# Performance work log

Measured on AMD Instinct MI355X. Metric: run time of the kernel, lower is better.

The kernel has to match this reference:

```python
import jax, jax.numpy as jnp
import numpy as np

N_NODES = 50000
N_EDGES = 800000
D_IN = 96
D_OUT = 96


def setup_inputs() -> dict:
    key = jax.random.key(0)
    k1, k2, k3 = jax.random.split(key, 3)
    x = jax.random.normal(k1, (N_NODES, D_IN), dtype=jnp.float32)
    edge_index = jax.random.randint(k2, (2, N_EDGES), 0, N_NODES, dtype=jnp.int64)
    edge_weight = jnp.ones((N_EDGES,), dtype=jnp.float32)
    # Glorot-ish init for the linear weight, zero bias (as in PyG GCNConv)
    W = jax.random.normal(k3, (D_IN, D_OUT), dtype=jnp.float32) * (1.0 / np.sqrt(D_IN))
    b = jnp.zeros((D_OUT,), dtype=jnp.float32)
    return {"x": x, "edge_index": edge_index, "edge_weight": edge_weight, "W": W, "b": b}


def reference(x, edge_index, edge_weight, W, b):
    """PyG GCNConv: out = D^{-1/2} (A + I) D^{-1/2} (x @ W) + b."""
    N = x.shape[0]
    row, col = edge_index[0], edge_index[1]  # source -> target
    # add self loops with weight 1 (PyG default add_self_loops=True)
    loop = jnp.arange(N, dtype=edge_index.dtype)
    row = jnp.concatenate([row, loop])
    col = jnp.concatenate([col, loop])
    ew = jnp.concatenate([edge_weight, jnp.ones((N,), dtype=edge_weight.dtype)])
    # symmetric normalization based on (weighted) in-degree over col
    deg = jax.ops.segment_sum(ew, col, num_segments=N)  # [N]
    dinv = jnp.where(deg > 0, jax.lax.rsqrt(deg), 0.0)
    norm = dinv[row] * ew * dinv[col]  # [E+N]
    # linear transform first (small GEMM), then gather-scale-scatter over edges
    h = x @ W  # [N, D_OUT]
    msg = h[row] * norm[:, None]  # [E+N, D_OUT]
    out = jax.ops.segment_sum(msg, col, num_segments=N)  # [N, D_OUT]
    return out + b
```

## Files before the change

kernel.cpp:

```cpp
#include <hip/hip_runtime.h>

#define N_NODES 50000
#define N_EDGES 800000
#define D 96
#define NBKT 512
#define BNODES 98
#define BCAP 2304
#define PART_B 250
#define EPB 3200
#define EPT 13
#define CAP 48
#define NSLOT (BNODES * CAP)
#define GCAP 768

typedef float vfloat4 __attribute__((ext_vector_type(4)));

__device__ __forceinline__ float bf_lo(unsigned u) { return __uint_as_float(u << 16); }
__device__ __forceinline__ float bf_hi(unsigned u) { return __uint_as_float(u & 0xFFFF0000u); }
__device__ __forceinline__ unsigned f2bf_bits(unsigned u) {
    return (u + 0x7FFFu + ((u >> 16) & 1u)) & 0xFFFF0000u;
}
__device__ __forceinline__ unsigned short f2bf16(float f) {
    return (unsigned short)(f2bf_bits(__float_as_uint(f)) >> 16);
}

__device__ __forceinline__ int exscan256(int v, int* wsum) {
    int lane = threadIdx.x & 63;
    int wave = threadIdx.x >> 6;
    int incl = v;
#pragma unroll
    for (int off = 1; off < 64; off <<= 1) {
        int t = __shfl_up(incl, off);
        if (lane >= off) incl += t;
    }
    if (lane == 63) wsum[wave] = incl;
    __syncthreads();
    int base = 0;
#pragma unroll
    for (int wv = 0; wv < 3; ++wv) base += (wv < wave) ? wsum[wv] : 0;
    return base + incl - v;
}

__global__ __launch_bounds__(256) void k_part(const int* __restrict__ row,
                                              const int* __restrict__ col,
                                              const float* __restrict__ ew,
                                              int* __restrict__ bkt_cnt,
                                              uint2* __restrict__ bktbuf) {
    __shared__ int hist[NBKT];
    __shared__ int cur[NBKT];
    int tid = threadIdx.x;
    hist[tid] = 0;
    hist[tid + 256] = 0;
    __syncthreads();
    int e0 = blockIdx.x * EPB;
    int myc[EPT];
#pragma unroll
    for (int k = 0; k < EPT; ++k) {
        int i = tid + 256 * k;
        myc[k] = (i < EPB) ? col[e0 + i] : -1;
    }
#pragma unroll
    for (int k = 0; k < EPT; ++k)
        if (myc[k] >= 0) atomicAdd(&hist[myc[k] / BNODES], 1);
    __syncthreads();
    cur[tid] = atomicAdd(&bkt_cnt[tid], hist[tid]);
    cur[tid + 256] = atomicAdd(&bkt_cnt[tid + 256], hist[tid + 256]);
    __syncthreads();
#pragma unroll
    for (int k = 0; k < EPT; ++k) {
        int i = tid + 256 * k;
        if (myc[k] >= 0) {
            int e = e0 + i;
            int c = myc[k];
            int b = c / BNODES;
            int p = atomicAdd(&cur[b], 1);
            if (p < BCAP)
                bktbuf[(size_t)b * BCAP + p] =
                    make_uint2((unsigned)row[e] | ((unsigned)(c - b * BNODES) << 16),
                               __float_as_uint(ew[e]));
        }
    }
}

__global__ __launch_bounds__(256) void k_bin(const int* __restrict__ bkt_cnt,
                                             const uint2* __restrict__ bktbuf,
                                             unsigned* __restrict__ recs,
                                             int* __restrict__ rowptr,
                                             float* __restrict__ dinv) {
    __shared__ int wsum1[4];
    __shared__ int wsum2[4];
    __shared__ int sbkt[NBKT];
    __shared__ int lcnt[BNODES];
    __shared__ int loff[256];
    __shared__ unsigned lslot[NSLOT];
    int tid = threadIdx.x;
    int b = blockIdx.x;

    int c0 = min(bkt_cnt[2 * tid], BCAP);
    int c1 = min(bkt_cnt[2 * tid + 1], BCAP);
    int ps = exscan256(c0 + c1, wsum1);
    sbkt[2 * tid] = ps;
    sbkt[2 * tid + 1] = ps + c0;
    if (tid < BNODES) lcnt[tid] = 0;
    __syncthreads();
    int gbase = sbkt[b];
    int ne = min(bkt_cnt[b], BCAP);

    for (int i = tid; i < ne; i += 256) {
        uint2 r = bktbuf[(size_t)b * BCAP + i];
        int lc = (int)(r.x >> 16);
        int p = atomicAdd(&lcnt[lc], 1);
        if (p < CAP) lslot[lc * CAP + p] = f2bf_bits(r.y) | (r.x & 0xFFFFu);
    }
    __syncthreads();

    int myv = (tid < BNODES) ? min(lcnt[tid], CAP) : 0;
    int ex2 = exscan256(myv, wsum2);
    loff[tid] = ex2;
    __syncthreads();

    for (int i = tid; i < NSLOT; i += 256) {
        int ln = i / CAP, s = i % CAP;
        if (s < min(lcnt[ln], CAP))
            recs[gbase + loff[ln] + s] = lslot[i];
    }
    int base = b * BNODES;
    if (tid < BNODES) {
        int n = base + tid;
        if (n <= N_NODES) rowptr[n] = gbase + loff[tid];
        if (n < N_NODES) {
            int cn = min(lcnt[tid], CAP);
            float d = 1.0f;
            for (int k = 0; k < cn; ++k) d += bf_hi(lslot[tid * CAP + k]);
            dinv[n] = rsqrtf(d);
        }
    }
}

__global__ __launch_bounds__(256) void k_gemm(const float* __restrict__ x,
                                              const float* __restrict__ W,
                                              const float* __restrict__ dinv,
                                              unsigned short* __restrict__ hb) {
    __shared__ float Wl[D * D];
    int tid = threadIdx.x;
    const float4* Wg4 = (const float4*)W;
    float4* Wl4 = (float4*)Wl;
    for (int i = tid; i < D * D / 4; i += 256) Wl4[i] = Wg4[i];
    __syncthreads();

    int jg = tid % 24;
    int ng = tid / 24;
    if (ng >= 10) return;
    int j = jg * 4;
    int node0 = blockIdx.x * 40 + ng * 4;

    float acc[4][4] = {};
    for (int k4 = 0; k4 < D / 4; ++k4) {
        vfloat4 xv[4];
#pragma unroll
        for (int i = 0; i < 4; ++i)
            xv[i] = __builtin_nontemporal_load(
                (const vfloat4*)&x[(node0 + i) * D + k4 * 4]);
#pragma unroll
        for (int kk = 0; kk < 4; ++kk) {
            float4 w4 = *(const float4*)&Wl[(k4 * 4 + kk) * D + j];
#pragma unroll
            for (int i = 0; i < 4; ++i) {
                float xs = (kk == 0) ? xv[i].x : (kk == 1) ? xv[i].y
                         : (kk == 2) ? xv[i].z : xv[i].w;
                acc[i][0] += xs * w4.x;
                acc[i][1] += xs * w4.y;
                acc[i][2] += xs * w4.z;
                acc[i][3] += xs * w4.w;
            }
        }
    }
#pragma unroll
    for (int i = 0; i < 4; ++i) {
        int n = node0 + i;
        float di = dinv[n];
        ushort4 pk;
        pk.x = f2bf16(acc[i][0] * di);
        pk.y = f2bf16(acc[i][1] * di);
        pk.z = f2bf16(acc[i][2] * di);
        pk.w = f2bf16(acc[i][3] * di);
        *(ushort4*)&hb[(size_t)n * D + j] = pk;
    }
}

__global__ __launch_bounds__(192) void k_gather(const int* __restrict__ rowptr,
                                                const unsigned* __restrict__ recs,
                                                const unsigned short* __restrict__ hb,
                                                const float* __restrict__ dinv,
                                                const float* __restrict__ bias,
                                                float* __restrict__ out) {
    __shared__ unsigned sre[GCAP];
    __shared__ int sptr[17];
    int tid = threadIdx.x;
    int nb = blockIdx.x * 16;

    if (tid < 17) sptr[tid] = rowptr[nb + tid];
    __syncthreads();
    int e0 = sptr[0];
    int stage = sptr[16] - e0;
    for (int i = tid; i < stage; i += 192) sre[i] = recs[e0 + i];
    __syncthreads();

    int local = tid / 12;
    int jq = tid % 12;
    int n = nb + local;
    int j = jq * 8;

    uint4 sv = *(const uint4*)(hb + (size_t)n * D + j);
    float acc[8];
    acc[0] = bf_lo(sv.x); acc[1] = bf_hi(sv.x);
    acc[2] = bf_lo(sv.y); acc[3] = bf_hi(sv.y);
    acc[4] = bf_lo(sv.z); acc[5] = bf_hi(sv.z);
    acc[6] = bf_lo(sv.w); acc[7] = bf_hi(sv.w);

    int ls = sptr[local] - e0;
    int le = sptr[local + 1] - e0;
    int idx = ls;
    for (; idx + 4 <= le; idx += 4) {
        unsigned r0 = sre[idx], r1 = sre[idx + 1], r2 = sre[idx + 2], r3 = sre[idx + 3];
        uint4 v0 = *(const uint4*)(hb + (size_t)(r0 & 0xFFFFu) * D + j);
        uint4 v1 = *(const uint4*)(hb + (size_t)(r1 & 0xFFFFu) * D + j);
        uint4 v2 = *(const uint4*)(hb + (size_t)(r2 & 0xFFFFu) * D + j);
        uint4 v3 = *(const uint4*)(hb + (size_t)(r3 & 0xFFFFu) * D + j);
        float w0 = bf_hi(r0), w1 = bf_hi(r1), w2 = bf_hi(r2), w3 = bf_hi(r3);
        acc[0] += w0 * bf_lo(v0.x); acc[1] += w0 * bf_hi(v0.x);
        acc[2] += w0 * bf_lo(v0.y); acc[3] += w0 * bf_hi(v0.y);
        acc[4] += w0 * bf_lo(v0.z); acc[5] += w0 * bf_hi(v0.z);
        acc[6] += w0 * bf_lo(v0.w); acc[7] += w0 * bf_hi(v0.w);
        acc[0] += w1 * bf_lo(v1.x); acc[1] += w1 * bf_hi(v1.x);
        acc[2] += w1 * bf_lo(v1.y); acc[3] += w1 * bf_hi(v1.y);
        acc[4] += w1 * bf_lo(v1.z); acc[5] += w1 * bf_hi(v1.z);
        acc[6] += w1 * bf_lo(v1.w); acc[7] += w1 * bf_hi(v1.w);
        acc[0] += w2 * bf_lo(v2.x); acc[1] += w2 * bf_hi(v2.x);
        acc[2] += w2 * bf_lo(v2.y); acc[3] += w2 * bf_hi(v2.y);
        acc[4] += w2 * bf_lo(v2.z); acc[5] += w2 * bf_hi(v2.z);
        acc[6] += w2 * bf_lo(v2.w); acc[7] += w2 * bf_hi(v2.w);
        acc[0] += w3 * bf_lo(v3.x); acc[1] += w3 * bf_hi(v3.x);
        acc[2] += w3 * bf_lo(v3.y); acc[3] += w3 * bf_hi(v3.y);
        acc[4] += w3 * bf_lo(v3.z); acc[5] += w3 * bf_hi(v3.z);
        acc[6] += w3 * bf_lo(v3.w); acc[7] += w3 * bf_hi(v3.w);
    }
    for (; idx < le; ++idx) {
        unsigned r0 = sre[idx];
        uint4 v0 = *(const uint4*)(hb + (size_t)(r0 & 0xFFFFu) * D + j);
        float w0 = bf_hi(r0);
        acc[0] += w0 * bf_lo(v0.x); acc[1] += w0 * bf_hi(v0.x);
        acc[2] += w0 * bf_lo(v0.y); acc[3] += w0 * bf_hi(v0.y);
        acc[4] += w0 * bf_lo(v0.z); acc[5] += w0 * bf_hi(v0.z);
        acc[6] += w0 * bf_lo(v0.w); acc[7] += w0 * bf_hi(v0.w);
    }

    float di = dinv[n];
    float4 b0 = *(const float4*)&bias[j];
    float4 b1 = *(const float4*)&bias[j + 4];
    vfloat4 o0, o1;
    o0.x = acc[0] * di + b0.x; o0.y = acc[1] * di + b0.y;
    o0.z = acc[2] * di + b0.z; o0.w = acc[3] * di + b0.w;
    o1.x = acc[4] * di + b1.x; o1.y = acc[5] * di + b1.y;
    o1.z = acc[6] * di + b1.z; o1.w = acc[7] * di + b1.w;
    __builtin_nontemporal_store(o0, (vfloat4*)&out[(size_t)n * D + j]);
    __builtin_nontemporal_store(o1, (vfloat4*)&out[(size_t)n * D + j + 4]);
}

extern "C" void kernel_launch(void* const* d_in, const int* in_sizes, int n_in,
                              void* d_out, int out_size, void* d_ws, size_t ws_size,
                              hipStream_t stream) {
    const float* x  = (const float*)d_in[0];
    const int*   ei = (const int*)d_in[1];
    const float* ew = (const float*)d_in[2];
    const float* W  = (const float*)d_in[3];
    const float* b  = (const float*)d_in[4];
    float* out = (float*)d_out;

    const int* row = ei;
    const int* col = ei + N_EDGES;

    char* p = (char*)d_ws;
    unsigned short* hb     = (unsigned short*)p;
    uint2*          bktbuf = (uint2*)p;            p += (size_t)N_NODES * D * 2;
    unsigned*       recs   = (unsigned*)p;         p += (size_t)N_EDGES * 4;
    int*            rowptr = (int*)p;              p += (size_t)(N_NODES + 16) * 4;
    float*          dinv   = (float*)p;            p += (size_t)N_NODES * 4;
    int*            bkt_cnt= (int*)p;              p += (size_t)NBKT * 4;

    (void)hipMemsetAsync(bkt_cnt, 0, NBKT * sizeof(int), stream);
    k_part  <<<PART_B, 256, 0, stream>>>(row, col, ew, bkt_cnt, bktbuf);
    k_bin   <<<NBKT, 256, 0, stream>>>(bkt_cnt, bktbuf, recs, rowptr, dinv);
    k_gemm  <<<1250, 256, 0, stream>>>(x, W, dinv, hb);
    k_gather<<<(N_NODES + 15) / 16, 192, 0, stream>>>(rowptr, recs, hb, dinv, b, out);
}
```

Measured before the change: 152.4 us.

## Sort nodes by degree within each bucket to balance gather warps

In the binning kernel, nodes within each bucket are now counting-sorted by in-degree and laid out in that order, producing a permuted rowptr and a perm array. The gather kernel processes nodes in this degree-sorted order, so the 16 nodes sharing a block (and the threads in a wavefront) have similar edge counts, which reduces divergence and idle lanes in the gather loop. In exchange, k_bin does extra shared-memory histogram and scan work, the gather launches over padded positions that exit early for padding nodes, and output writes become scattered by the permutation.

```diff
diff --git a/kernel.cpp b/kernel.cpp
--- a/kernel.cpp
+++ b/kernel.cpp
@@ -5,6 +5,7 @@
 #define D 96
 #define NBKT 512
 #define BNODES 98
+#define N_GPOS (NBKT * BNODES)
 #define BCAP 2304
 #define PART_B 250
 #define EPB 3200
@@ -85,13 +86,18 @@
 __global__ __launch_bounds__(256) void k_bin(const int* __restrict__ bkt_cnt,
                                              const uint2* __restrict__ bktbuf,
                                              unsigned* __restrict__ recs,
-                                             int* __restrict__ rowptr,
+                                             int* __restrict__ srowptr,
+                                             int* __restrict__ perm,
                                              float* __restrict__ dinv) {
     __shared__ int wsum1[4];
-    __shared__ int wsum2[4];
     __shared__ int sbkt[NBKT];
     __shared__ int lcnt[BNODES];
-    __shared__ int loff[256];
+    __shared__ int sdeg[BNODES];
+    __shared__ int sloff[BNODES];
+    __shared__ int cntd[CAP + 1];
+    __shared__ int nodebase[CAP + 1];
+    __shared__ int edgebase[CAP + 1];
+    __shared__ int rankctr[CAP + 1];
     __shared__ unsigned lslot[NSLOT];
     int tid = threadIdx.x;
     int b = blockIdx.x;
@@ -102,6 +108,7 @@
     sbkt[2 * tid] = ps;
     sbkt[2 * tid + 1] = ps + c0;
     if (tid < BNODES) lcnt[tid] = 0;
+    if (tid <= CAP) { cntd[tid] = 0; rankctr[tid] = 0; }
     __syncthreads();
     int gbase = sbkt[b];
     int ne = min(bkt_cnt[b], BCAP);
@@ -114,26 +121,50 @@
     }
     __syncthreads();
 
-    int myv = (tid < BNODES) ? min(lcnt[tid], CAP) : 0;
-    int ex2 = exscan256(myv, wsum2);
-    loff[tid] = ex2;
+    if (tid < BNODES) {
+        int dg = min(lcnt[tid], CAP);
+        sdeg[tid] = dg;
+        atomicAdd(&cntd[dg], 1);
+    }
+    __syncthreads();
+
+    if (tid < 64) {
+        int d = (tid <= CAP) ? cntd[tid] : 0;
+        int e = (tid <= CAP) ? d * tid : 0;
+        int di = d, ei = e;
+#pragma unroll
+        for (int off = 1; off < 64; off <<= 1) {
+            int td = __shfl_up(di, off);
+            int te = __shfl_up(ei, off);
+            if (tid >= off) { di += td; ei += te; }
+        }
+        if (tid <= CAP) { nodebase[tid] = di - d; edgebase[tid] = ei - e; }
+    }
+    __syncthreads();
+
+    if (tid < BNODES) {
+        int dg = sdeg[tid];
+        int r = atomicAdd(&rankctr[dg], 1);
+        int spos = nodebase[dg] + r;
+        int eoff = edgebase[dg] + r * dg;
+        sloff[tid] = eoff;
+        int gpos = b * BNODES + spos;
+        int n = b * BNODES + tid;
+        perm[gpos] = (n < N_NODES) ? n : -1;
+        srowptr[gpos] = gbase + eoff;
+        if (n < N_NODES) {
+            float d = 1.0f;
+            for (int k = 0; k < dg; ++k) d += bf_hi(lslot[tid * CAP + k]);
+            dinv[n] = rsqrtf(d);
+        }
+    }
+    if (b == NBKT - 1 && tid == 0)
+        srowptr[N_GPOS] = gbase + edgebase[CAP] + cntd[CAP] * CAP;
     __syncthreads();
 
     for (int i = tid; i < NSLOT; i += 256) {
         int ln = i / CAP, s = i % CAP;
-        if (s < min(lcnt[ln], CAP))
-            recs[gbase + loff[ln] + s] = lslot[i];
-    }
-    int base = b * BNODES;
-    if (tid < BNODES) {
-        int n = base + tid;
-        if (n <= N_NODES) rowptr[n] = gbase + loff[tid];
-        if (n < N_NODES) {
-            int cn = min(lcnt[tid], CAP);
-            float d = 1.0f;
-            for (int k = 0; k < cn; ++k) d += bf_hi(lslot[tid * CAP + k]);
-            dinv[n] = rsqrtf(d);
-        }
+        if (s < sdeg[ln]) recs[gbase + sloff[ln] + s] = lslot[i];
     }
 }
 
@@ -188,7 +219,8 @@
     }
 }
 
-__global__ __launch_bounds__(192) void k_gather(const int* __restrict__ rowptr,
+__global__ __launch_bounds__(192) void k_gather(const int* __restrict__ srowptr,
+                                                const int* __restrict__ perm,
                                                 const unsigned* __restrict__ recs,
                                                 const unsigned short* __restrict__ hb,
                                                 const float* __restrict__ dinv,
@@ -196,10 +228,12 @@
                                                 float* __restrict__ out) {
     __shared__ unsigned sre[GCAP];
     __shared__ int sptr[17];
+    __shared__ int spn[16];
     int tid = threadIdx.x;
     int nb = blockIdx.x * 16;
 
-    if (tid < 17) sptr[tid] = rowptr[nb + tid];
+    if (tid < 17) sptr[tid] = srowptr[nb + tid];
+    if (tid >= 32 && tid < 48) spn[tid - 32] = perm[nb + tid - 32];
     __syncthreads();
     int e0 = sptr[0];
     int stage = sptr[16] - e0;
@@ -208,10 +242,11 @@
 
     int local = tid / 12;
     int jq = tid % 12;
-    int n = nb + local;
+    int pn = spn[local];
+    if (pn < 0) return;
     int j = jq * 8;
 
-    uint4 sv = *(const uint4*)(hb + (size_t)n * D + j);
+    uint4 sv = *(const uint4*)(hb + (size_t)pn * D + j);
     float acc[8];
     acc[0] = bf_lo(sv.x); acc[1] = bf_hi(sv.x);
     acc[2] = bf_lo(sv.y); acc[3] = bf_hi(sv.y);
@@ -255,7 +290,7 @@
         acc[6] += w0 * bf_lo(v0.w); acc[7] += w0 * bf_hi(v0.w);
     }
 
-    float di = dinv[n];
+    float di = dinv[pn];
     float4 b0 = *(const float4*)&bias[j];
     float4 b1 = *(const float4*)&bias[j + 4];
     vfloat4 o0, o1;
@@ -263,8 +298,8 @@
     o0.z = acc[2] * di + b0.z; o0.w = acc[3] * di + b0.w;
     o1.x = acc[4] * di + b1.x; o1.y = acc[5] * di + b1.y;
     o1.z = acc[6] * di + b1.z; o1.w = acc[7] * di + b1.w;
-    __builtin_nontemporal_store(o0, (vfloat4*)&out[(size_t)n * D + j]);
-    __builtin_nontemporal_store(o1, (vfloat4*)&out[(size_t)n * D + j + 4]);
+    __builtin_nontemporal_store(o0, (vfloat4*)&out[(size_t)pn * D + j]);
+    __builtin_nontemporal_store(o1, (vfloat4*)&out[(size_t)pn * D + j + 4]);
 }
 
 extern "C" void kernel_launch(void* const* d_in, const int* in_sizes, int n_in,
@@ -284,13 +319,14 @@
     unsigned short* hb     = (unsigned short*)p;
     uint2*          bktbuf = (uint2*)p;            p += (size_t)N_NODES * D * 2;
     unsigned*       recs   = (unsigned*)p;         p += (size_t)N_EDGES * 4;
-    int*            rowptr = (int*)p;              p += (size_t)(N_NODES + 16) * 4;
+    int*            srowptr= (int*)p;              p += (size_t)(N_GPOS + 16) * 4;
+    int*            perm   = (int*)p;              p += (size_t)N_GPOS * 4;
     float*          dinv   = (float*)p;            p += (size_t)N_NODES * 4;
     int*            bkt_cnt= (int*)p;              p += (size_t)NBKT * 4;
 
     (void)hipMemsetAsync(bkt_cnt, 0, NBKT * sizeof(int), stream);
     k_part  <<<PART_B, 256, 0, stream>>>(row, col, ew, bkt_cnt, bktbuf);
-    k_bin   <<<NBKT, 256, 0, stream>>>(bkt_cnt, bktbuf, recs, rowptr, dinv);
+    k_bin   <<<NBKT, 256, 0, stream>>>(bkt_cnt, bktbuf, recs, srowptr, perm, dinv);
     k_gemm  <<<1250, 256, 0, stream>>>(x, W, dinv, hb);
-    k_gather<<<(N_NODES + 15) / 16, 192, 0, stream>>>(rowptr, recs, hb, dinv, b, out);
-}
+    k_gather<<<N_GPOS / 16, 192, 0, stream>>>(srowptr, perm, recs, hb, dinv, b, out);
+}
```

Result: no change. 153.5 us (+0.7%).

## Replace CSR build and gather with per-bucket LDS atomic scatter

Applied to the files above, without the earlier changes.

Drops the binning kernel that built a CSR (recs/rowptr) and replaces it with a lightweight degree kernel that accumulates per-bucket degrees with LDS float atomics. The gather kernel becomes a per-bucket scatter: each of 512 blocks reads its bucket's edges directly, gathers bf16 source rows and accumulates into a 98x98 float LDS tile via shared-memory atomics, then writes normalized output with the self-loop and bias added. This removes a CSR compaction pass and its global traffic. In exchange it adds heavy LDS atomic contention, uses only 21 groups of 12 threads per block, and runs just 512 large blocks with about 38 KB of LDS each, so occupancy and latency hiding are lower. It also removes the old 48-edge-per-node cap, although the bucket-capacity cap of 2304 edges remains.

```diff
diff --git a/kernel.cpp b/kernel.cpp
--- a/kernel.cpp
+++ b/kernel.cpp
@@ -5,13 +5,11 @@
 #define D 96
 #define NBKT 512
 #define BNODES 98
+#define SROW 98
 #define BCAP 2304
 #define PART_B 250
 #define EPB 3200
 #define EPT 13
-#define CAP 48
-#define NSLOT (BNODES * CAP)
-#define GCAP 768
 
 typedef float vfloat4 __attribute__((ext_vector_type(4)));
 
@@ -22,23 +20,6 @@
 }
 __device__ __forceinline__ unsigned short f2bf16(float f) {
     return (unsigned short)(f2bf_bits(__float_as_uint(f)) >> 16);
-}
-
-__device__ __forceinline__ int exscan256(int v, int* wsum) {
-    int lane = threadIdx.x & 63;
-    int wave = threadIdx.x >> 6;
-    int incl = v;
-#pragma unroll
-    for (int off = 1; off < 64; off <<= 1) {
-        int t = __shfl_up(incl, off);
-        if (lane >= off) incl += t;
-    }
-    if (lane == 63) wsum[wave] = incl;
-    __syncthreads();
-    int base = 0;
-#pragma unroll
-    for (int wv = 0; wv < 3; ++wv) base += (wv < wave) ? wsum[wv] : 0;
-    return base + incl - v;
 }
 
 __global__ __launch_bounds__(256) void k_part(const int* __restrict__ row,
@@ -82,58 +63,23 @@
     }
 }
 
-__global__ __launch_bounds__(256) void k_bin(const int* __restrict__ bkt_cnt,
+__global__ __launch_bounds__(256) void k_deg(const int* __restrict__ bkt_cnt,
                                              const uint2* __restrict__ bktbuf,
-                                             unsigned* __restrict__ recs,
-                                             int* __restrict__ rowptr,
                                              float* __restrict__ dinv) {
-    __shared__ int wsum1[4];
-    __shared__ int wsum2[4];
-    __shared__ int sbkt[NBKT];
-    __shared__ int lcnt[BNODES];
-    __shared__ int loff[256];
-    __shared__ unsigned lslot[NSLOT];
+    __shared__ float ldeg[BNODES];
     int tid = threadIdx.x;
     int b = blockIdx.x;
-
-    int c0 = min(bkt_cnt[2 * tid], BCAP);
-    int c1 = min(bkt_cnt[2 * tid + 1], BCAP);
-    int ps = exscan256(c0 + c1, wsum1);
-    sbkt[2 * tid] = ps;
-    sbkt[2 * tid + 1] = ps + c0;
-    if (tid < BNODES) lcnt[tid] = 0;
-    __syncthreads();
-    int gbase = sbkt[b];
+    if (tid < BNODES) ldeg[tid] = 1.0f;
+    __syncthreads();
     int ne = min(bkt_cnt[b], BCAP);
-
     for (int i = tid; i < ne; i += 256) {
         uint2 r = bktbuf[(size_t)b * BCAP + i];
-        int lc = (int)(r.x >> 16);
-        int p = atomicAdd(&lcnt[lc], 1);
-        if (p < CAP) lslot[lc * CAP + p] = f2bf_bits(r.y) | (r.x & 0xFFFFu);
-    }
-    __syncthreads();
-
-    int myv = (tid < BNODES) ? min(lcnt[tid], CAP) : 0;
-    int ex2 = exscan256(myv, wsum2);
-    loff[tid] = ex2;
-    __syncthreads();
-
-    for (int i = tid; i < NSLOT; i += 256) {
-        int ln = i / CAP, s = i % CAP;
-        if (s < min(lcnt[ln], CAP))
-            recs[gbase + loff[ln] + s] = lslot[i];
-    }
-    int base = b * BNODES;
+        atomicAdd(&ldeg[r.x >> 16], __uint_as_float(r.y));
+    }
+    __syncthreads();
     if (tid < BNODES) {
-        int n = base + tid;
-        if (n <= N_NODES) rowptr[n] = gbase + loff[tid];
-        if (n < N_NODES) {
-            int cn = min(lcnt[tid], CAP);
-            float d = 1.0f;
-            for (int k = 0; k < cn; ++k) d += bf_hi(lslot[tid * CAP + k]);
-            dinv[n] = rsqrtf(d);
-        }
+        int n = b * BNODES + tid;
+        if (n < N_NODES) dinv[n] = rsqrtf(ldeg[tid]);
     }
 }
 
@@ -188,83 +134,66 @@
     }
 }
 
-__global__ __launch_bounds__(192) void k_gather(const int* __restrict__ rowptr,
-                                                const unsigned* __restrict__ recs,
-                                                const unsigned short* __restrict__ hb,
-                                                const float* __restrict__ dinv,
-                                                const float* __restrict__ bias,
-                                                float* __restrict__ out) {
-    __shared__ unsigned sre[GCAP];
-    __shared__ int sptr[17];
-    int tid = threadIdx.x;
-    int nb = blockIdx.x * 16;
-
-    if (tid < 17) sptr[tid] = rowptr[nb + tid];
-    __syncthreads();
-    int e0 = sptr[0];
-    int stage = sptr[16] - e0;
-    for (int i = tid; i < stage; i += 192) sre[i] = recs[e0 + i];
-    __syncthreads();
-
-    int local = tid / 12;
-    int jq = tid % 12;
-    int n = nb + local;
-    int j = jq * 8;
-
-    uint4 sv = *(const uint4*)(hb + (size_t)n * D + j);
-    float acc[8];
-    acc[0] = bf_lo(sv.x); acc[1] = bf_hi(sv.x);
-    acc[2] = bf_lo(sv.y); acc[3] = bf_hi(sv.y);
-    acc[4] = bf_lo(sv.z); acc[5] = bf_hi(sv.z);
-    acc[6] = bf_lo(sv.w); acc[7] = bf_hi(sv.w);
-
-    int ls = sptr[local] - e0;
-    int le = sptr[local + 1] - e0;
-    int idx = ls;
-    for (; idx + 4 <= le; idx += 4) {
-        unsigned r0 = sre[idx], r1 = sre[idx + 1], r2 = sre[idx + 2], r3 = sre[idx + 3];
-        uint4 v0 = *(const uint4*)(hb + (size_t)(r0 & 0xFFFFu) * D + j);
-        uint4 v1 = *(const uint4*)(hb + (size_t)(r1 & 0xFFFFu) * D + j);
-        uint4 v2 = *(const uint4*)(hb + (size_t)(r2 & 0xFFFFu) * D + j);
-        uint4 v3 = *(const uint4*)(hb + (size_t)(r3 & 0xFFFFu) * D + j);
-        float w0 = bf_hi(r0), w1 = bf_hi(r1), w2 = bf_hi(r2), w3 = bf_hi(r3);
-        acc[0] += w0 * bf_lo(v0.x); acc[1] += w0 * bf_hi(v0.x);
-        acc[2] += w0 * bf_lo(v0.y); acc[3] += w0 * bf_hi(v0.y);
-        acc[4] += w0 * bf_lo(v0.z); acc[5] += w0 * bf_hi(v0.z);
-        acc[6] += w0 * bf_lo(v0.w); acc[7] += w0 * bf_hi(v0.w);
-        acc[0] += w1 * bf_lo(v1.x); acc[1] += w1 * bf_hi(v1.x);
-        acc[2] += w1 * bf_lo(v1.y); acc[3] += w1 * bf_hi(v1.y);
-        acc[4] += w1 * bf_lo(v1.z); acc[5] += w1 * bf_hi(v1.z);
-        acc[6] += w1 * bf_lo(v1.w); acc[7] += w1 * bf_hi(v1.w);
-        acc[0] += w2 * bf_lo(v2.x); acc[1] += w2 * bf_hi(v2.x);
-        acc[2] += w2 * bf_lo(v2.y); acc[3] += w2 * bf_hi(v2.y);
-        acc[4] += w2 * bf_lo(v2.z); acc[5] += w2 * bf_hi(v2.z);
-        acc[6] += w2 * bf_lo(v2.w); acc[7] += w2 * bf_hi(v2.w);
-        acc[0] += w3 * bf_lo(v3.x); acc[1] += w3 * bf_hi(v3.x);
-        acc[2] += w3 * bf_lo(v3.y); acc[3] += w3 * bf_hi(v3.y);
-        acc[4] += w3 * bf_lo(v3.z); acc[5] += w3 * bf_hi(v3.z);
-        acc[6] += w3 * bf_lo(v3.w); acc[7] += w3 * bf_hi(v3.w);
-    }
-    for (; idx < le; ++idx) {
-        unsigned r0 = sre[idx];
-        uint4 v0 = *(const uint4*)(hb + (size_t)(r0 & 0xFFFFu) * D + j);
-        float w0 = bf_hi(r0);
-        acc[0] += w0 * bf_lo(v0.x); acc[1] += w0 * bf_hi(v0.x);
-        acc[2] += w0 * bf_lo(v0.y); acc[3] += w0 * bf_hi(v0.y);
-        acc[4] += w0 * bf_lo(v0.z); acc[5] += w0 * bf_hi(v0.z);
-        acc[6] += w0 * bf_lo(v0.w); acc[7] += w0 * bf_hi(v0.w);
-    }
-
-    float di = dinv[n];
-    float4 b0 = *(const float4*)&bias[j];
-    float4 b1 = *(const float4*)&bias[j + 4];
-    vfloat4 o0, o1;
-    o0.x = acc[0] * di + b0.x; o0.y = acc[1] * di + b0.y;
-    o0.z = acc[2] * di + b0.z; o0.w = acc[3] * di + b0.w;
-    o1.x = acc[4] * di + b1.x; o1.y = acc[5] * di + b1.y;
-    o1.z = acc[6] * di + b1.z; o1.w = acc[7] * di + b1.w;
-    __builtin_nontemporal_store(o0, (vfloat4*)&out[(size_t)n * D + j]);
-    __builtin_nontemporal_store(o1, (vfloat4*)&out[(size_t)n * D + j + 4]);
+__global__ __launch_bounds__(256) void k_scat(const int* __restrict__ bkt_cnt,
+                                              const uint2* __restrict__ bktbuf,
+                                              const unsigned short* __restrict__ hb,
+                                              const float* __restrict__ dinv,
+                                              const float* __restrict__ bias,
+                                              float* __restrict__ out) {
+    __shared__ float acc[BNODES * SROW];
+    int tid = threadIdx.x;
+    int b = blockIdx.x;
+    for (int i = tid; i < BNODES * SROW; i += 256) acc[i] = 0.0f;
+    __syncthreads();
+
+    int ne = min(bkt_cnt[b], BCAP);
+    int g = tid / 12;
+    int l = tid % 12;
+    int j = l * 8;
+
+    if (g < 21) {
+        const uint2* eb = bktbuf + (size_t)b * BCAP;
+        for (int i = g; i < ne; i += 21) {
+            uint2 r = eb[i];
+            int src = (int)(r.x & 0xFFFFu);
+            int lc = (int)(r.x >> 16);
+            float w = __uint_as_float(r.y);
+            uint4 v = *(const uint4*)(hb + (size_t)src * D + j);
+            float* dp = &acc[lc * SROW + j];
+            atomicAdd(dp + 0, w * bf_lo(v.x));
+            atomicAdd(dp + 1, w * bf_hi(v.x));
+            atomicAdd(dp + 2, w * bf_lo(v.y));
+            atomicAdd(dp + 3, w * bf_hi(v.y));
+            atomicAdd(dp + 4, w * bf_lo(v.z));
+            atomicAdd(dp + 5, w * bf_hi(v.z));
+            atomicAdd(dp + 6, w * bf_lo(v.w));
+            atomicAdd(dp + 7, w * bf_hi(v.w));
+        }
+    }
+    __syncthreads();
+
+    if (g < 21) {
+        float4 b0 = *(const float4*)&bias[j];
+        float4 b1 = *(const float4*)&bias[j + 4];
+        for (int ln = g; ln < BNODES; ln += 21) {
+            int n = b * BNODES + ln;
+            if (n >= N_NODES) continue;
+            float di = dinv[n];
+            uint4 sv = *(const uint4*)(hb + (size_t)n * D + j);
+            const float* ap = &acc[ln * SROW + j];
+            vfloat4 o0, o1;
+            o0.x = (ap[0] + bf_lo(sv.x)) * di + b0.x;
+            o0.y = (ap[1] + bf_hi(sv.x)) * di + b0.y;
+            o0.z = (ap[2] + bf_lo(sv.y)) * di + b0.z;
+            o0.w = (ap[3] + bf_hi(sv.y)) * di + b0.w;
+            o1.x = (ap[4] + bf_lo(sv.z)) * di + b1.x;
+            o1.y = (ap[5] + bf_hi(sv.z)) * di + b1.y;
+            o1.z = (ap[6] + bf_lo(sv.w)) * di + b1.z;
+            o1.w = (ap[7] + bf_hi(sv.w)) * di + b1.w;
+            __builtin_nontemporal_store(o0, (vfloat4*)&out[(size_t)n * D + j]);
+            __builtin_nontemporal_store(o1, (vfloat4*)&out[(size_t)n * D + j + 4]);
+        }
+    }
 }
 
 extern "C" void kernel_launch(void* const* d_in, const int* in_sizes, int n_in,
@@ -281,16 +210,14 @@
     const int* col = ei + N_EDGES;
 
     char* p = (char*)d_ws;
-    unsigned short* hb     = (unsigned short*)p;
-    uint2*          bktbuf = (uint2*)p;            p += (size_t)N_NODES * D * 2;
-    unsigned*       recs   = (unsigned*)p;         p += (size_t)N_EDGES * 4;
-    int*            rowptr = (int*)p;              p += (size_t)(N_NODES + 16) * 4;
+    unsigned short* hb     = (unsigned short*)p;   p += (size_t)N_NODES * D * 2;
+    uint2*          bktbuf = (uint2*)p;            p += (size_t)NBKT * BCAP * 8;
     float*          dinv   = (float*)p;            p += (size_t)N_NODES * 4;
     int*            bkt_cnt= (int*)p;              p += (size_t)NBKT * 4;
 
     (void)hipMemsetAsync(bkt_cnt, 0, NBKT * sizeof(int), stream);
-    k_part  <<<PART_B, 256, 0, stream>>>(row, col, ew, bkt_cnt, bktbuf);
-    k_bin   <<<NBKT, 256, 0, stream>>>(bkt_cnt, bktbuf, recs, rowptr, dinv);
-    k_gemm  <<<1250, 256, 0, stream>>>(x, W, dinv, hb);
-    k_gather<<<(N_NODES + 15) / 16, 192, 0, stream>>>(rowptr, recs, hb, dinv, b, out);
-}
+    k_part<<<PART_B, 256, 0, stream>>>(row, col, ew, bkt_cnt, bktbuf);
+    k_deg <<<NBKT, 256, 0, stream>>>(bkt_cnt, bktbuf, dinv);
+    k_gemm<<<1250, 256, 0, stream>>>(x, W, dinv, hb);
+    k_scat<<<NBKT, 256, 0, stream>>>(bkt_cnt, bktbuf, hb, dinv, b, out);
+}
```

After: 526.3 us. 3.45x slower.
